# Kernel tuning notes

Measured on AMD Instinct MI355X. Metric: run time of the kernel, lower is better.

The kernel has to match this reference:

```python
import jax, jax.numpy as jnp
import numpy as np
import math

B, D, N, M = 8, 64, 4096, 4096


def setup_inputs() -> dict:
    key = jax.random.key(0)
    k1, k2, k3, k4 = jax.random.split(key, 4)
    return {
        "src_embedding": jax.random.normal(k1, (B, D, N), dtype=jnp.float32),
        "tgt_embedding": jax.random.normal(k2, (B, D, M), dtype=jnp.float32),
        "src": jax.random.normal(k3, (B, 3, N), dtype=jnp.float32),
        "tgt": jax.random.normal(k4, (B, 3, M), dtype=jnp.float32),
    }


def reference(src_embedding, tgt_embedding, src, tgt):
    d_k = src_embedding.shape[1]
    # scores: [B, N, M] = src_emb^T @ tgt_emb / sqrt(d)
    scores = jnp.einsum("bdn,bdm->bnm", src_embedding, tgt_embedding) / jnp.sqrt(
        jnp.asarray(d_k, dtype=src_embedding.dtype)
    )
    attn = jax.nn.softmax(scores, axis=2)  # softmax over target points M
    # src_corr: [B, 3, N] = tgt @ attn^T  (soft correspondence of each src point)
    src_corr = jnp.einsum("bcm,bnm->bcn", tgt, attn)
    return (src, src_corr)
```

## Files before the change

### kernel.cpp

```cpp
#include <hip/hip_runtime.h>
#include <hip/hip_bf16.h>

#define B_ 8
#define D_ 64
#define N_ 4096
#define M_ 4096
#define B3N (B_*3*N_)

#define SCALE2 0.18033688011112042f

typedef short bf16x8 __attribute__((ext_vector_type(8)));
typedef float f32x4 __attribute__((ext_vector_type(4)));
typedef __fp16 half2v __attribute__((ext_vector_type(2)));
typedef __fp16 half4v __attribute__((ext_vector_type(4)));
typedef unsigned int uint4v __attribute__((ext_vector_type(4)));

#if __has_builtin(__builtin_amdgcn_exp2f)
#define EXP2(x) __builtin_amdgcn_exp2f(x)
#else
#define EXP2(x) exp2f(x)
#endif

__device__ __forceinline__ unsigned fbits(float f) { return __builtin_bit_cast(unsigned, f); }

__device__ __forceinline__ unsigned pkbf(float hi, float lo) {
#if __has_builtin(__builtin_amdgcn_perm)
    return __builtin_amdgcn_perm(fbits(hi), fbits(lo), 0x07060302u);
#else
    return (fbits(hi) & 0xFFFF0000u) | (fbits(lo) >> 16);
#endif
}

__device__ __forceinline__ half2v pkhalf(float a, float b) {
#if __has_builtin(__builtin_amdgcn_cvt_pkrtz)
    return __builtin_bit_cast(half2v, __builtin_amdgcn_cvt_pkrtz(a, b));
#else
    half2v r; r[0] = (__fp16)a; r[1] = (__fp16)b; return r;
#endif
}

#define MFMA_PV(a,b,c) __builtin_amdgcn_mfma_f32_16x16x16f16((a),(b),(c),0,0,0)


__global__ __launch_bounds__(64) void prep_swz_kernel(const float* __restrict__ qe,
                                                      const float* __restrict__ ke,
                                                      unsigned short* __restrict__ qs,
                                                      unsigned short* __restrict__ ks)
{
    int blk = blockIdx.x;
    bool isq = blk >= 512;
    int l  = blk & 511;
    int b  = l >> 6;
    int p  = ((l & 63) << 6) + threadIdx.x;
    const float* ip = (isq ? qe : ke) + (size_t)b * D_ * M_ + p;
    unsigned short* op = (isq ? qs : ks) + (size_t)b * M_ * D_
                       + (size_t)(p >> 4) * 1024 + (p & 15) * 8;
    float sc = isq ? SCALE2 : 1.0f;
    #pragma unroll
    for (int i = 0; i < 8; ++i) {
        float v[8];
        #pragma unroll
        for (int d = 0; d < 8; ++d) v[d] = ip[(size_t)(8*i + d) * M_] * sc;
        uint4v w;
        #pragma unroll
        for (int j = 0; j < 4; ++j) w[j] = pkbf(v[2*j+1], v[2*j]);
        *(uint4v*)(op + (i>>2)*512 + (i&3)*128) = w;
    }
}

__global__ __launch_bounds__(256) void prep3_kernel(const float4* __restrict__ src4,
                                                    const float* __restrict__ tgt,
                                                    float4* __restrict__ out4,
                                                    __fp16* __restrict__ thswz)
{
    int blk = blockIdx.x;
    if (blk < 96) {
        int i = blk*256 + threadIdx.x;
        out4[i] = src4[i];
        return;
    }
    int unit = (blk - 96)*4 + (threadIdx.x >> 6);
    int b = unit >> 8, mblk = unit & 255;
    int l = threadIdx.x & 63;
    int c = l & 3, g = l >> 4;
    int m = mblk*16 + 4*g;
    float4 tv;
    if (c < 3) tv = *(const float4*)(tgt + ((size_t)b*3 + c)*M_ + m);
    else       tv = make_float4(1.f, 1.f, 1.f, 1.f);
    half2v a01 = pkhalf(tv.x, tv.y);
    half2v a23 = pkhalf(tv.z, tv.w);
    half4v af = __builtin_shufflevector(a01, a23, 0, 1, 2, 3);
    *(half4v*)((char*)thswz + (size_t)unit*512 + l*8) = af;
}

template<int S>
__global__ __launch_bounds__(256, 4)
void attn8_kernel(const unsigned short* __restrict__ qswz,
                  const unsigned short* __restrict__ kswz,
                  const __fp16* __restrict__ thswz,
                  float* __restrict__ partials)
{
    __shared__ __align__(16) unsigned char kbuf[2][4096];
    __shared__ __align__(16) unsigned char abuf[2][1024];

    const int lane = threadIdx.x & 63;
    const int wave = threadIdx.x >> 6;
    const int lm = lane & 15, g = lane >> 4;
    const int b = blockIdx.z, slice = blockIdx.y;
    const int n0 = blockIdx.x * 256 + wave * 64;
    const int mchunk = M_ / S, mbase = slice * mchunk;

    const char* qp = (const char*)qswz
                   + ((size_t)b * N_ * D_ + (size_t)(n0 >> 4) * 1024) * 2;
    bf16x8 qf[4][2];
    #pragma unroll
    for (int f = 0; f < 4; ++f) {
        qf[f][0] = *(const bf16x8*)(qp + f*2048 + lane*16);
        qf[f][1] = *(const bf16x8*)(qp + f*2048 + 1024 + lane*16);
    }

    const char* kp = (const char*)kswz
                   + ((size_t)b * M_ * D_ + (size_t)(mbase >> 4) * 1024) * 2;
    const char* tp = (const char*)thswz
                   + ((size_t)b * (M_/16) + (size_t)(mbase >> 4)) * 512;

    {
        bf16x8 k0 = *(const bf16x8*)(kp + wave*1024 + lane*16);
        *(bf16x8*)(kbuf[0] + wave*1024 + lane*16) = k0;
        if (wave == 0) {
            uint4v a0 = *(const uint4v*)(tp + lane*16);
            *(uint4v*)(abuf[0] + lane*16) = a0;
        }
    }
    __syncthreads();

    f32x4 D2[4] = {{0,0,0,0},{0,0,0,0},{0,0,0,0},{0,0,0,0}};

    auto compute = [&](bf16x8 kA, bf16x8 kB, half4v aF) {
        #pragma unroll
        for (int f = 0; f < 4; ++f) {
            f32x4 c4 = {0,0,0,0};
            c4 = __builtin_amdgcn_mfma_f32_16x16x32_bf16(kA, qf[f][0], c4, 0, 0, 0);
            c4 = __builtin_amdgcn_mfma_f32_16x16x32_bf16(kB, qf[f][1], c4, 0, 0, 0);
            float e0 = EXP2(c4[0]);
            float e1 = EXP2(c4[1]);
            float e2 = EXP2(c4[2]);
            float e3 = EXP2(c4[3]);
            half2v p01 = pkhalf(e0, e1);
            half2v p23 = pkhalf(e2, e3);
            half4v pbf = __builtin_shufflevector(p01, p23, 0, 1, 2, 3);
            D2[f] = MFMA_PV(aF, pbf, D2[f]);
        }
    };

    int cur = 0;
    const int iters = mchunk / 32;
    for (int it = 0; it < iters; ++it) {
        bf16x8 knxt;
        uint4v anxt;
        const bool more = (it < iters - 1);
        if (more) {
            knxt = *(const bf16x8*)(kp + 4096 + wave*1024 + lane*16);
            if (wave == 0) anxt = *(const uint4v*)(tp + 1024 + lane*16);
        }
        bf16x8 ka0 = *(const bf16x8*)(kbuf[cur] + 0*1024 + lane*16);
        bf16x8 kb0 = *(const bf16x8*)(kbuf[cur] + 1*1024 + lane*16);
        bf16x8 ka1 = *(const bf16x8*)(kbuf[cur] + 2*1024 + lane*16);
        bf16x8 kb1 = *(const bf16x8*)(kbuf[cur] + 3*1024 + lane*16);
        half4v af0 = *(const half4v*)(abuf[cur] + lane*8);
        half4v af1 = *(const half4v*)(abuf[cur] + 512 + lane*8);

        compute(ka0, kb0, af0);
        compute(ka1, kb1, af1);

        if (more) {
            *(bf16x8*)(kbuf[cur^1] + wave*1024 + lane*16) = knxt;
            if (wave == 0) *(uint4v*)(abuf[cur^1] + lane*16) = anxt;
            kp += 4096; tp += 1024;
        }
        __syncthreads();
        cur ^= 1;
    }

    {
        size_t base = ((size_t)slice * B_ + b) * 4 * N_ + (size_t)g * N_;
        const int sel = (g + 3) & 3;
        #pragma unroll
        for (int f = 0; f < 4; ++f)
            partials[base + n0 + 16*f + lm] = D2[f][sel];
    }
}

__global__ __launch_bounds__(64) void prep_kernel(const float* __restrict__ qe,
                                                  const float* __restrict__ ke,
                                                  unsigned short* __restrict__ qb,
                                                  unsigned short* __restrict__ kb)
{
    int blk = blockIdx.x;
    bool isq = blk >= 512;
    int l  = blk & 511;
    int b  = l >> 6;
    int p  = ((l & 63) << 6) + threadIdx.x;
    const float* ip = (isq ? qe : ke) + (size_t)b * D_ * M_ + p;
    unsigned short* op = (isq ? qb : kb) + ((size_t)b * M_ + p) * D_;
    float sc = isq ? SCALE2 : 1.0f;
    #pragma unroll
    for (int i = 0; i < 8; ++i) {
        float v[8];
        #pragma unroll
        for (int d = 0; d < 8; ++d) v[d] = ip[(size_t)(8*i + d) * M_] * sc;
        uint4v w;
        #pragma unroll
        for (int j = 0; j < 4; ++j) w[j] = pkbf(v[2*j+1], v[2*j]);
        *(uint4v*)(op + 8*i) = w;
    }
}

template<int S>
__global__ __launch_bounds__(64, 4)
void attn2_kernel(const unsigned short* __restrict__ qb,
                  const unsigned short* __restrict__ kb,
                  const float* __restrict__ tgt,
                  float* __restrict__ partials)
{
    const int t  = threadIdx.x, lm = t & 15, g = t >> 4;
    const int b  = blockIdx.z, slice = blockIdx.y, n0 = blockIdx.x * 64;
    const int mchunk = M_ / S, mbase = slice * mchunk;

    bf16x8 qf[4][2];
    #pragma unroll
    for (int f = 0; f < 4; ++f) {
        const unsigned short* qrow = qb + ((size_t)b * N_ + n0 + 16*f + lm) * D_ + 8*g;
        qf[f][0] = *(const bf16x8*)(qrow);
        qf[f][1] = *(const bf16x8*)(qrow + 32);
    }

    const bool isones = (lm & 3) == 3;
    const int  c_ld   = isones ? 2 : (lm & 3);
    half2v one2 = pkhalf(1.0f, 1.0f);
    const half4v ones4 = __builtin_shufflevector(one2, one2, 0, 1, 0, 1);

    const unsigned short* krow = kb + ((size_t)b * M_ + mbase + lm) * D_ + 8*g;
    const float* tp = tgt + ((size_t)b * 3 + c_ld) * M_ + mbase + 4*g;

    f32x4 D2[4] = {{0,0,0,0},{0,0,0,0},{0,0,0,0},{0,0,0,0}};

    for (int ms = 0; ms < mchunk; ms += 16) {
        bf16x8 ka  = *(const bf16x8*)(krow);
        bf16x8 kb8 = *(const bf16x8*)(krow + 32);
        f32x4 tv = *(const f32x4*)(tp);
        half2v a01 = pkhalf(tv[0], tv[1]);
        half2v a23 = pkhalf(tv[2], tv[3]);
        half4v afr = __builtin_shufflevector(a01, a23, 0, 1, 2, 3);
        afr = isones ? ones4 : afr;

        #pragma unroll
        for (int f = 0; f < 4; ++f) {
            f32x4 c4 = {0,0,0,0};
            c4 = __builtin_amdgcn_mfma_f32_16x16x32_bf16(ka,  qf[f][0], c4, 0, 0, 0);
            c4 = __builtin_amdgcn_mfma_f32_16x16x32_bf16(kb8, qf[f][1], c4, 0, 0, 0);
            float e0 = EXP2(c4[0]);
            float e1 = EXP2(c4[1]);
            float e2 = EXP2(c4[2]);
            float e3 = EXP2(c4[3]);
            half2v p01 = pkhalf(e0, e1);
            half2v p23 = pkhalf(e2, e3);
            half4v pbf = __builtin_shufflevector(p01, p23, 0, 1, 2, 3);
            D2[f] = MFMA_PV(afr, pbf, D2[f]);
        }
        krow += 16 * D_;
        tp   += 16;
    }

    if (t < 16) {
        size_t base = ((size_t)slice * B_ + b) * 4 * N_;
        #pragma unroll
        for (int f = 0; f < 4; ++f) {
            int n = n0 + 16*f + t;
            partials[base + 0*N_ + n] = D2[f][3];
            partials[base + 1*N_ + n] = D2[f][0];
            partials[base + 2*N_ + n] = D2[f][1];
            partials[base + 3*N_ + n] = D2[f][2];
        }
    }
}

__global__ void copy_kernel(const float4* __restrict__ src, float4* __restrict__ out) {
    int i = blockIdx.x*256 + threadIdx.x;
    out[i] = src[i];
}

template<int S>
__global__ void finalize_kernel(const float* __restrict__ ws, float* __restrict__ out) {
    int tid = blockIdx.x*256 + threadIdx.x;
    int b = tid >> 12;
    int n = tid & (N_-1);
    float den = 0.f, x = 0.f, y = 0.f, z = 0.f;
    #pragma unroll
    for (int s = 0; s < S; ++s) {
        size_t base = ((size_t)s*B_ + b)*4*N_ + n;
        den += ws[base];
        x   += ws[base + 1*N_];
        y   += ws[base + 2*N_];
        z   += ws[base + 3*N_];
    }
    float inv = 1.0f/den;
    out[B3N + ((size_t)b*3 + 0)*N_ + n] = x*inv;
    out[B3N + ((size_t)b*3 + 1)*N_ + n] = y*inv;
    out[B3N + ((size_t)b*3 + 2)*N_ + n] = z*inv;
}

extern "C" void kernel_launch(void* const* d_in, const int* in_sizes, int n_in,
                              void* d_out, int out_size, void* d_ws, size_t ws_size,
                              hipStream_t stream) {
    const float* qe  = (const float*)d_in[0];
    const float* ke  = (const float*)d_in[1];
    const float* src = (const float*)d_in[2];
    const float* tg  = (const float*)d_in[3];
    float* out = (float*)d_out;

    const size_t embElems = (size_t)B_ * M_ * D_;
    const size_t embBytes = 2 * embElems * 2;
    const size_t thBytes  = (size_t)B_ * 256 * 512;
    const size_t partB8   = (size_t)8 * B_ * 4 * N_ * 4;
    const size_t needSwz  = embBytes + thBytes + partB8;
    const size_t needOld  = embBytes + partB8;

    unsigned short* kb16 = (unsigned short*)d_ws;
    unsigned short* qb16 = kb16 + embElems;
    __fp16* thswz = (__fp16*)((char*)d_ws + embBytes);
    float* partialsNew = (float*)((char*)d_ws + embBytes + thBytes);
    float* partialsOld = (float*)((char*)d_ws + embBytes);

    if (ws_size >= needSwz) {
        prep_swz_kernel<<<1024, 64, 0, stream>>>(qe, ke, qb16, kb16);
        prep3_kernel<<<608, 256, 0, stream>>>((const float4*)src, tg, (float4*)out, thswz);
        dim3 grid(N_/256, 8, B_);
        attn8_kernel<8><<<grid, 256, 0, stream>>>(qb16, kb16, thswz, partialsNew);
        finalize_kernel<8><<<(B_*N_)/256, 256, 0, stream>>>(partialsNew, out);
    } else if (ws_size >= needOld) {
        copy_kernel<<<96, 256, 0, stream>>>((const float4*)src, (float4*)out);
        prep_kernel<<<1024, 64, 0, stream>>>(qe, ke, qb16, kb16);
        dim3 grid(N_/64, 8, B_);
        attn2_kernel<8><<<grid, 64, 0, stream>>>(qb16, kb16, tg, partialsOld);
        finalize_kernel<8><<<(B_*N_)/256, 256, 0, stream>>>(partialsOld, out);
    }
}
```

Measured before the change: 37.69 us.

## Stream K tiles via direct global-to-LDS loads in larger rounds

Replaces the register-staged K tile double buffer with direct global_load_lds transfers into LDS. Each round now covers 128 key columns instead of 32, which cuts the number of block barriers by a factor of four. The attention-weight tile (thswz) is read straight from global memory instead of being staged through LDS. This uses more LDS (32KB per block), which may lower occupancy, and it relies on the async LDS loads being complete at the barrier.

```diff
diff --git a/kernel.cpp b/kernel.cpp
--- a/kernel.cpp
+++ b/kernel.cpp
@@ -40,6 +40,13 @@
 }
 
 #define MFMA_PV(a,b,c) __builtin_amdgcn_mfma_f32_16x16x16f16((a),(b),(c),0,0,0)
+
+__device__ __forceinline__ void gload_lds16(const void* g, void* lds) {
+    __builtin_amdgcn_global_load_lds(
+        (const __attribute__((address_space(1))) unsigned int*)g,
+        (__attribute__((address_space(3))) unsigned int*)(unsigned)(unsigned long long)lds,
+        16, 0, 0);
+}
 
 
 __global__ __launch_bounds__(64) void prep_swz_kernel(const float* __restrict__ qe,
@@ -95,13 +102,12 @@
 
 template<int S>
 __global__ __launch_bounds__(256, 4)
-void attn8_kernel(const unsigned short* __restrict__ qswz,
+void attn9_kernel(const unsigned short* __restrict__ qswz,
                   const unsigned short* __restrict__ kswz,
                   const __fp16* __restrict__ thswz,
                   float* __restrict__ partials)
 {
-    __shared__ __align__(16) unsigned char kbuf[2][4096];
-    __shared__ __align__(16) unsigned char abuf[2][1024];
+    __shared__ __align__(16) unsigned char kbuf[2][16384];
 
     const int lane = threadIdx.x & 63;
     const int wave = threadIdx.x >> 6;
@@ -120,18 +126,14 @@
     }
 
     const char* kp = (const char*)kswz
-                   + ((size_t)b * M_ * D_ + (size_t)(mbase >> 4) * 1024) * 2;
+                   + ((size_t)b * M_ * D_ + (size_t)(mbase >> 4) * 1024) * 2
+                   + lane*16;
     const char* tp = (const char*)thswz
                    + ((size_t)b * (M_/16) + (size_t)(mbase >> 4)) * 512;
 
-    {
-        bf16x8 k0 = *(const bf16x8*)(kp + wave*1024 + lane*16);
-        *(bf16x8*)(kbuf[0] + wave*1024 + lane*16) = k0;
-        if (wave == 0) {
-            uint4v a0 = *(const uint4v*)(tp + lane*16);
-            *(uint4v*)(abuf[0] + lane*16) = a0;
-        }
-    }
+    #pragma unroll
+    for (int i = 0; i < 4; ++i)
+        gload_lds16(kp + wave*4096 + i*1024, kbuf[0] + wave*4096 + i*1024);
     __syncthreads();
 
     f32x4 D2[4] = {{0,0,0,0},{0,0,0,0},{0,0,0,0},{0,0,0,0}};
@@ -154,29 +156,26 @@
     };
 
     int cur = 0;
-    const int iters = mchunk / 32;
-    for (int it = 0; it < iters; ++it) {
-        bf16x8 knxt;
-        uint4v anxt;
-        const bool more = (it < iters - 1);
-        if (more) {
-            knxt = *(const bf16x8*)(kp + 4096 + wave*1024 + lane*16);
-            if (wave == 0) anxt = *(const uint4v*)(tp + 1024 + lane*16);
-        }
-        bf16x8 ka0 = *(const bf16x8*)(kbuf[cur] + 0*1024 + lane*16);
-        bf16x8 kb0 = *(const bf16x8*)(kbuf[cur] + 1*1024 + lane*16);
-        bf16x8 ka1 = *(const bf16x8*)(kbuf[cur] + 2*1024 + lane*16);
-        bf16x8 kb1 = *(const bf16x8*)(kbuf[cur] + 3*1024 + lane*16);
-        half4v af0 = *(const half4v*)(abuf[cur] + lane*8);
-        half4v af1 = *(const half4v*)(abuf[cur] + 512 + lane*8);
-
-        compute(ka0, kb0, af0);
-        compute(ka1, kb1, af1);
-
-        if (more) {
-            *(bf16x8*)(kbuf[cur^1] + wave*1024 + lane*16) = knxt;
-            if (wave == 0) *(uint4v*)(abuf[cur^1] + lane*16) = anxt;
-            kp += 4096; tp += 1024;
+    const int rounds = mchunk / 128;
+    for (int r = 0; r < rounds; ++r) {
+        if (r < rounds - 1) {
+            const char* ksrc = kp + (r+1)*16384 + wave*4096;
+            #pragma unroll
+            for (int i = 0; i < 4; ++i)
+                gload_lds16(ksrc + i*1024, kbuf[cur^1] + wave*4096 + i*1024);
+        }
+        #pragma unroll
+        for (int it = 0; it < 4; ++it) {
+            const unsigned char* kb4 = kbuf[cur] + it*4096;
+            bf16x8 ka0 = *(const bf16x8*)(kb4 + 0*1024 + lane*16);
+            bf16x8 kb0 = *(const bf16x8*)(kb4 + 1*1024 + lane*16);
+            bf16x8 ka1 = *(const bf16x8*)(kb4 + 2*1024 + lane*16);
+            bf16x8 kb1 = *(const bf16x8*)(kb4 + 3*1024 + lane*16);
+            const char* tpi = tp + (r*4 + it)*1024;
+            half4v af0 = *(const half4v*)(tpi + lane*8);
+            half4v af1 = *(const half4v*)(tpi + 512 + lane*8);
+            compute(ka0, kb0, af0);
+            compute(ka1, kb1, af1);
         }
         __syncthreads();
         cur ^= 1;
@@ -336,7 +335,7 @@
         prep_swz_kernel<<<1024, 64, 0, stream>>>(qe, ke, qb16, kb16);
         prep3_kernel<<<608, 256, 0, stream>>>((const float4*)src, tg, (float4*)out, thswz);
         dim3 grid(N_/256, 8, B_);
-        attn8_kernel<8><<<grid, 256, 0, stream>>>(qb16, kb16, thswz, partialsNew);
+        attn9_kernel<8><<<grid, 256, 0, stream>>>(qb16, kb16, thswz, partialsNew);
         finalize_kernel<8><<<(B_*N_)/256, 256, 0, stream>>>(partialsNew, out);
     } else if (ws_size >= needOld) {
         copy_kernel<<<96, 256, 0, stream>>>((const float4*)src, (float4*)out);
```

Result: no change. 37.93 us (+0.6%).
